# Optimization experiments

Measured on AMD Instinct MI355X. Metric: run time of the kernel, lower is better.

The kernel has to match this reference:

```python
import jax, jax.numpy as jnp
import numpy as np

PAD_IDX = 0
EPS = 1e-5


def make_pos(L):
    # phrase[i, j] = j - i, i.e. row i is range(-i, L-i)
    phrase = (np.arange(L)[None, :] - np.arange(L)[:, None]).astype(np.float32)
    half = int(np.ceil(L / 2))
    freq = np.linspace(0.0, L, L, dtype=np.float32)[1:half]          # [F]
    pos = freq[:, None, None] * phrase[None] / L * 2.0 * np.pi       # [F, L, L]
    pos = np.concatenate([np.cos(pos), np.sin(pos)], axis=0)        # [2F, L, L]
    return jnp.asarray(np.transpose(pos, (1, 0, 2)))                # [L, P=2F, L]


def setup_inputs() -> dict:
    key = jax.random.key(0)
    ks = jax.random.split(key, 8)
    B, L, V, D, H = 2048, 64, 4096, 64, 8
    P = 2 * (int(np.ceil(L / 2)) - 1)  # 62
    inputs = jax.random.randint(ks[0], (B, L), 0, V)
    W_emb = jax.random.normal(ks[1], (V, D), jnp.float32) * 0.02
    W_emb = W_emb.at[PAD_IDX].set(0.0)  # padding_idx row is zero
    W_qkv = jax.random.normal(ks[2], (3 * H * D, D), jnp.float32) * 0.02
    W_pos = jax.random.normal(ks[3], (P, L), jnp.float32) * 0.02
    ln_g = jnp.ones((D,), jnp.float32)
    ln_b = jnp.zeros((D,), jnp.float32)
    W1 = jax.random.normal(ks[4], (64, H), jnp.float32) * 0.1
    b1 = jnp.zeros((64,), jnp.float32)
    W2 = jax.random.normal(ks[5], (32, 64), jnp.float32) * 0.1
    b2 = jnp.zeros((32,), jnp.float32)
    return dict(inputs=inputs, W_emb=W_emb, W_qkv=W_qkv, W_pos=W_pos,
                ln_g=ln_g, ln_b=ln_b, W1=W1, b1=b1, W2=W2, b2=b2,
                n_words=4, n_names=16)


def reference(inputs, W_emb, W_qkv, W_pos, ln_g, ln_b, W1, b1, W2, b2, n_words, n_names):
    B, L = inputs.shape
    V, D = W_emb.shape
    H = W_qkv.shape[0] // (3 * D)
    pos = make_pos(L)  # [L, P, L]
    P = pos.shape[1]

    # compute_qkv: per-char q/k/v tables, then gather per token.
    qkv = (W_emb @ W_qkv.T).reshape(V, 3 * H, D)
    q, k, v = qkv[:, :H], qkv[:, H:2 * H], qkv[:, 2 * H:]
    q_t = jnp.take(q, inputs, axis=0)  # [B, L, H, D]
    k_t = jnp.take(k, inputs, axis=0)
    v_t = jnp.take(v, inputs, axis=0)

    # Equivalent to gathering char_sim[h, ids, ids]: qkv is a per-token linear,
    # so q[ids] @ k[ids]^T == char_sim.index_select(1, ids).index_select(-1, ids).
    sim = jnp.einsum('blhd,bmhd->bhlm', q_t, k_t) / jnp.sqrt(jnp.float32(D))
    key_pad = (inputs == PAD_IDX)[:, None, None, :]
    sim = jnp.where(key_pad, jnp.float32(-1e9), sim)  # char_sim[:, :, pad_idx] = -1e9

    # positional bias: Linear(L->P) on clipped scores, contracted with pos basis.
    sim_clip = jnp.where(sim > -1e8, sim, jnp.float32(0.0))
    pos_w = jnp.einsum('bhlm,pm->bhlp', sim_clip, W_pos)        # [B, H, L, P]
    pos_bias = jnp.einsum('bhlp,lpm->bhlm', pos_w, pos) / P     # mean over P

    attn = jax.nn.softmax(sim + pos_bias, axis=-1)              # dropout p=0 -> id
    out = jnp.einsum('bhlm,bmhd->blhd', attn, v_t)              # [B, L, H, D]

    # sdpa LayerNorm over word_vec_d
    mu = out.mean(-1, keepdims=True)
    var = out.var(-1, keepdims=True)
    out = (out - mu) * jax.lax.rsqrt(var + EPS) * ln_g + ln_b

    # MLP over the head dimension: [B, L, D, H] -> [B, L, D, 32]
    ft = jnp.swapaxes(out, 2, 3)
    h1 = jax.nn.relu(jnp.einsum('bldh,oh->bldo', ft, W1) + b1)
    h2 = jnp.einsum('bldo,po->bldp', h1, W2) + b2
    char_ft = h2.reshape(B, L, -1)                              # [B, L, D*32]

    # masked mean pooling over chars -> word feature
    maskf = (inputs != PAD_IDX).astype(char_ft.dtype)
    word_ft = jnp.einsum('bl,blf->bf', maskf, char_ft) / maskf.sum(-1, keepdims=True)

    # equal-size splits: words -> names (mean) -> groups of names
    Fdim = word_ft.shape[-1]
    name_ft = word_ft.reshape(B // n_words, n_words, Fdim).mean(1)
    return name_ft.reshape(-1, n_names, Fdim)
```

## Files before the change

### kernel.cpp

```cpp
#include <hip/hip_runtime.h>
#include <hip/hip_bf16.h>


typedef __attribute__((ext_vector_type(8))) short short8;
typedef __attribute__((ext_vector_type(4))) float f32x4;

union FragU { uint4 u; short8 v; };

__device__ __forceinline__ unsigned short f2bf(float f) {
    union { float f; unsigned int i; } c; c.f = f;
    unsigned int i = c.i;
    unsigned int r = (i + 0x7fffu + ((i >> 16) & 1u)) >> 16;
    return (unsigned short)r;
}
__device__ __forceinline__ float asf(unsigned int u) {
    union { unsigned int i; float f; } c; c.i = u; return c.f;
}
__device__ __forceinline__ float bfsel(uint2 g, int i) {
    unsigned u = (i < 2) ? g.x : g.y;
    return asf((i & 1) ? (u & 0xffff0000u) : (u << 16));
}
__device__ __forceinline__ unsigned cvtpk(float lo, float hi) {
    unsigned r;
    asm("v_cvt_pk_bf16_f32 %0, %1, %2" : "=v"(r) : "v"(lo), "v"(hi));
    return r;
}

__device__ __forceinline__ void packstore4(unsigned* rowptr, int c,
                                           float v0, float v1, float v2, float v3) {
    float p0 = __shfl_xor(v0, 1), p1 = __shfl_xor(v1, 1);
    float p2 = __shfl_xor(v2, 1), p3 = __shfl_xor(v3, 1);
    int odd = c & 1;
    float lo0 = odd ? p2 : v0, hi0 = odd ? v2 : p0;
    float lo1 = odd ? p3 : v1, hi1 = odd ? v3 : p1;
    unsigned a0 = cvtpk(lo0, hi0);
    unsigned a1 = cvtpk(lo1, hi1);
    int ba = (c >> 1) + (odd ? 16 : 0);
    rowptr[ba] = a0; rowptr[ba + 8] = a1;
}

__device__ __forceinline__ void packline(unsigned* rowbase, int c,
                                         float v0, float v1, float v2, float v3) {
    float p0 = __shfl_xor(v0, 1), p1 = __shfl_xor(v1, 1);
    float p2 = __shfl_xor(v2, 1), p3 = __shfl_xor(v3, 1);
    int odd = c & 1;
    float lo0 = odd ? p2 : v0, hi0 = odd ? v2 : p0;
    float lo1 = odd ? p3 : v1, hi1 = odd ? v3 : p1;
    unsigned a0 = cvtpk(lo0, hi0);
    unsigned a1 = cvtpk(lo1, hi1);
    int s = (c >> 1) + (odd ? 8 : 0);
    rowbase[s] = a0; rowbase[s + 16] = a1;
}

__global__ __launch_bounds__(256) void k_qkv(const float* __restrict__ W_emb,
                                             const float* __restrict__ W_qkv,
                                             unsigned short* __restrict__ qkvb) {
    __shared__ float At[4096];
    __shared__ float Bt[4096];
    int t = threadIdx.x;
    int bt = blockIdx.x / 24, rt = blockIdx.x - bt * 24;
    int r = t >> 2, part = t & 3;
    const float4* esrc = (const float4*)(W_emb + (size_t)((bt << 6) + r) * 64 + part * 16);
    const float4* wsrc = (const float4*)(W_qkv + (size_t)((rt << 6) + r) * 64 + part * 16);
#pragma unroll
    for (int j = 0; j < 4; ++j) {
        float4 e4 = esrc[j], w4 = wsrc[j];
        int c0 = part * 16 + j * 4;
        At[(c0 + 0) * 64 + r] = e4.x; At[(c0 + 1) * 64 + r] = e4.y;
        At[(c0 + 2) * 64 + r] = e4.z; At[(c0 + 3) * 64 + r] = e4.w;
        Bt[(c0 + 0) * 64 + r] = w4.x; Bt[(c0 + 1) * 64 + r] = w4.y;
        Bt[(c0 + 2) * 64 + r] = w4.z; Bt[(c0 + 3) * 64 + r] = w4.w;
    }
    __syncthreads();
    int l0 = (t >> 4) << 2, m0 = (t & 15) << 2;
    float acc[4][4] = {};
#pragma unroll 4
    for (int k = 0; k < 64; ++k) {
        float4 a  = *(const float4*)(At + k * 64 + l0);
        float4 bb = *(const float4*)(Bt + k * 64 + m0);
        float aa[4] = {a.x, a.y, a.z, a.w};
        float bv[4] = {bb.x, bb.y, bb.z, bb.w};
#pragma unroll
        for (int i = 0; i < 4; ++i)
#pragma unroll
            for (int j = 0; j < 4; ++j)
                acc[i][j] = fmaf(aa[i], bv[j], acc[i][j]);
    }
    float qs = (rt < 8) ? 0.18033688f : 1.0f;
#pragma unroll
    for (int i = 0; i < 4; ++i) {
        unsigned w0 = (unsigned)f2bf(acc[i][0] * qs) | ((unsigned)f2bf(acc[i][1] * qs) << 16);
        unsigned w1 = (unsigned)f2bf(acc[i][2] * qs) | ((unsigned)f2bf(acc[i][3] * qs) << 16);
        unsigned* dst = (unsigned*)(qkvb + (size_t)((bt << 6) + l0 + i) * 1536 + (rt << 6) + m0);
        dst[0] = w0; dst[1] = w1;
    }
}

__global__ void k_tab(const float* __restrict__ W_pos,
                      unsigned short* __restrict__ cst,
                      unsigned short* __restrict__ csl,
                      unsigned short* __restrict__ wpos) {
    int e = blockIdx.x * 256 + threadIdx.x;
    const float w = 6.283185307179586f / 63.0f;
    int row = e >> 6, col = e & 63;
    {
        int j = col, x = row;
        float val = 0.0f;
        if (j < 31)       val = cosf(w * (float)(((j + 1) * x) % 63));
        else if (j >= 32 && j < 63) val = sinf(w * (float)(((j - 31) * x) % 63));
        cst[e] = f2bf(val);
    }
    {
        int j = row, x = col;
        float val = 0.0f;
        if (j < 31)       val = cosf(w * (float)(((j + 1) * x) % 63));
        else if (j >= 32 && j < 63) val = sinf(w * (float)(((j - 31) * x) % 63));
        csl[e] = f2bf(val);
    }
    {
        int j = row;
        float val = 0.0f;
        if (j < 31) val = W_pos[j * 64 + col];
        else if (j >= 32 && j < 63) val = W_pos[(j - 1) * 64 + col];
        wpos[e] = f2bf(val);
    }
}

__global__ __launch_bounds__(128, 4) void k_attn(
    const int* __restrict__ inputs,
    const unsigned short* __restrict__ qkvb,
    const unsigned short* __restrict__ cstg,
    const unsigned short* __restrict__ cslg,
    const unsigned short* __restrict__ wposg,
    const float* __restrict__ ln_g,
    const float* __restrict__ ln_b,
    unsigned short* __restrict__ out_n)
{
    __shared__ __align__(16) unsigned int smem[4608];
    unsigned int* S0d = smem;
    unsigned int* S1d = smem + 2304;
    int t = threadIdx.x, w2 = t >> 6, lane = t & 63;
    int b = blockIdx.x >> 3, h = blockIdx.x & 7;
    const int* toks = inputs + b * 64;
    int r = lane & 15, q = lane >> 4, c = r;
    int tk = toks[lane];
    int mt0 = 2 * w2;
    const float INV62 = 1.0f / 62.0f;

    int mk[4]; float gvv[4], bvv[4];
#pragma unroll
    for (int nt = 0; nt < 4; ++nt) {
        mk[nt] = (toks[16 * nt + c] == 0);
        gvv[nt] = ln_g[16 * nt + c];
        bvv[nt] = ln_b[16 * nt + c];
    }

    {
        const uint4* src = (const uint4*)(qkvb + (size_t)tk * 1536 + (w2 ? 512 : 0) + h * 64);
        uint4* dst = (uint4*)((w2 ? S1d : S0d) + lane * 36);
#pragma unroll
        for (int j = 0; j < 8; ++j) dst[j] = src[j];
    }
    __syncthreads();

    f32x4 sc[2][4], acc[2][4];
    const f32x4 zf = {0.f, 0.f, 0.f, 0.f};

#pragma unroll
    for (int u = 0; u < 2; ++u)
#pragma unroll
        for (int nt = 0; nt < 4; ++nt) sc[u][nt] = zf;
#pragma unroll
    for (int ks = 0; ks < 2; ++ks) {
        FragU Af[2], Bf[4];
#pragma unroll
        for (int u = 0; u < 2; ++u)
            Af[u].u = *(const uint4*)(S0d + (16 * (mt0 + u) + r) * 36 + 16 * ks + 4 * q);
#pragma unroll
        for (int nt = 0; nt < 4; ++nt)
            Bf[nt].u = *(const uint4*)(S1d + (16 * nt + r) * 36 + 16 * ks + 4 * q);
#pragma unroll
        for (int u = 0; u < 2; ++u)
#pragma unroll
            for (int nt = 0; nt < 4; ++nt)
                sc[u][nt] = __builtin_amdgcn_mfma_f32_16x16x32_bf16(Af[u].v, Bf[nt].v, sc[u][nt], 0, 0, 0);
    }
#pragma unroll
    for (int u = 0; u < 2; ++u)
#pragma unroll
        for (int i = 0; i < 4; ++i) {
            int l = 16 * (mt0 + u) + 4 * q + i;
            packstore4(S0d + l * 36, c, sc[u][0][i], sc[u][1][i], sc[u][2][i], sc[u][3][i]);
        }
    __syncthreads();

#pragma unroll
    for (int u = 0; u < 2; ++u)
#pragma unroll
        for (int nt = 0; nt < 4; ++nt) acc[u][nt] = zf;
#pragma unroll
    for (int ks = 0; ks < 2; ++ks) {
        FragU Af[2], Bf[4];
#pragma unroll
        for (int u = 0; u < 2; ++u)
            Af[u].u = *(const uint4*)(S0d + (16 * (mt0 + u) + r) * 36 + 16 * ks + 4 * q);
#pragma unroll
        for (int nt = 0; nt < 4; ++nt)
            Bf[nt].u = *(const uint4*)(wposg + (16 * nt + r) * 64 + 32 * ks + 8 * q);
#pragma unroll
        for (int u = 0; u < 2; ++u)
#pragma unroll
            for (int nt = 0; nt < 4; ++nt)
                acc[u][nt] = __builtin_amdgcn_mfma_f32_16x16x32_bf16(Af[u].v, Bf[nt].v, acc[u][nt], 0, 0, 0);
    }
#pragma unroll
    for (int u = 0; u < 2; ++u) {
        int mt = mt0 + u;
        uint2 t00 = *(const uint2*)(cslg + (c) * 64 + 16 * mt + 4 * q);
        uint2 t01 = *(const uint2*)(cslg + (32 + c) * 64 + 16 * mt + 4 * q);
        uint2 t10 = *(const uint2*)(cslg + (16 + c) * 64 + 16 * mt + 4 * q);
        uint2 t11 = *(const uint2*)(cslg + (48 + c) * 64 + 16 * mt + 4 * q);
#pragma unroll
        for (int i = 0; i < 4; ++i) {
            int l = 16 * mt + 4 * q + i;
            float cv0 = bfsel(t00, i), sv0 = bfsel(t01, i);
            float cv1 = bfsel(t10, i), sv1 = bfsel(t11, i);
            float pc0 = acc[u][0][i], ps0 = acc[u][2][i];
            float pc1 = acc[u][1][i], ps1 = acc[u][3][i];
            float u0 = pc0 * cv0 - ps0 * sv0;
            float u1 = pc1 * cv1 - ps1 * sv1;
            float u2 = pc0 * sv0 + ps0 * cv0;
            float u3 = pc1 * sv1 + ps1 * cv1;
            packstore4(S1d + l * 36, c, u0, u1, u2, u3);
        }
    }

#pragma unroll
    for (int u = 0; u < 2; ++u)
#pragma unroll
        for (int nt = 0; nt < 4; ++nt) acc[u][nt] = zf;
#pragma unroll
    for (int ks = 0; ks < 2; ++ks) {
        FragU Af[2], Bf[4];
#pragma unroll
        for (int u = 0; u < 2; ++u)
            Af[u].u = *(const uint4*)(S1d + (16 * (mt0 + u) + r) * 36 + 16 * ks + 4 * q);
#pragma unroll
        for (int nt = 0; nt < 4; ++nt)
            Bf[nt].u = *(const uint4*)(cstg + (16 * nt + r) * 64 + 32 * ks + 8 * q);
#pragma unroll
        for (int u = 0; u < 2; ++u)
#pragma unroll
            for (int nt = 0; nt < 4; ++nt)
                acc[u][nt] = __builtin_amdgcn_mfma_f32_16x16x32_bf16(Af[u].v, Bf[nt].v, acc[u][nt], 0, 0, 0);
    }

    uint4 V4[4];
    {
        const uint4* vsrc = (const uint4*)(qkvb + (size_t)tk * 1536 + 1024 + h * 64 + 32 * w2);
#pragma unroll
        for (int j = 0; j < 4; ++j) V4[j] = vsrc[j];
    }

#pragma unroll
    for (int u = 0; u < 2; ++u)
#pragma unroll
        for (int i = 0; i < 4; ++i) {
            int l = 16 * (mt0 + u) + 4 * q + i;
            float e0 = mk[0] ? 0.f : __builtin_amdgcn_exp2f(fmaf(acc[u][0][i], INV62, sc[u][0][i]));
            float e1 = mk[1] ? 0.f : __builtin_amdgcn_exp2f(fmaf(acc[u][1][i], INV62, sc[u][1][i]));
            float e2 = mk[2] ? 0.f : __builtin_amdgcn_exp2f(fmaf(acc[u][2][i], INV62, sc[u][2][i]));
            float e3 = mk[3] ? 0.f : __builtin_amdgcn_exp2f(fmaf(acc[u][3][i], INV62, sc[u][3][i]));
            float s = e0 + e1 + e2 + e3;
            s += __shfl_xor(s, 1);
            s += __shfl_xor(s, 2);
            s += __shfl_xor(s, 4);
            s += __shfl_xor(s, 8);
            float inv = __builtin_amdgcn_rcpf(s);
            packstore4(S0d + l * 36, c, e0 * inv, e1 * inv, e2 * inv, e3 * inv);
        }

    {
        int odd = lane & 1;
        const unsigned* Vd = (const unsigned*)V4;
#pragma unroll
        for (int jj = 0; jj < 16; ++jj) {
            unsigned my = Vd[jj];
            unsigned pr = __shfl_xor(my, 1);
            unsigned val = odd ? ((pr >> 16) | (my & 0xffff0000u))
                               : ((my & 0xffffu) | (pr << 16));
            S1d[(32 * w2 + 2 * jj + odd) * 36 + (lane >> 1)] = val;
        }
    }
    __syncthreads();

#pragma unroll
    for (int u = 0; u < 2; ++u)
#pragma unroll
        for (int nt = 0; nt < 4; ++nt) acc[u][nt] = zf;
#pragma unroll
    for (int ks = 0; ks < 2; ++ks) {
        FragU Af[2], Bf[4];
#pragma unroll
        for (int u = 0; u < 2; ++u)
            Af[u].u = *(const uint4*)(S0d + (16 * (mt0 + u) + r) * 36 + 16 * ks + 4 * q);
#pragma unroll
        for (int nt = 0; nt < 4; ++nt)
            Bf[nt].u = *(const uint4*)(S1d + (16 * nt + r) * 36 + 16 * ks + 4 * q);
#pragma unroll
        for (int u = 0; u < 2; ++u)
#pragma unroll
            for (int nt = 0; nt < 4; ++nt)
                acc[u][nt] = __builtin_amdgcn_mfma_f32_16x16x32_bf16(Af[u].v, Bf[nt].v, acc[u][nt], 0, 0, 0);
    }
    {
        unsigned* outw = (unsigned*)out_n;
        size_t hb = ((size_t)b * 8 + h) * 64;
#pragma unroll
        for (int u = 0; u < 2; ++u)
#pragma unroll
            for (int i = 0; i < 4; ++i) {
                int l = 16 * (mt0 + u) + 4 * q + i;
                float v0 = acc[u][0][i], v1 = acc[u][1][i], v2 = acc[u][2][i], v3 = acc[u][3][i];
                float s1 = v0 + v1 + v2 + v3;
                float s2 = v0 * v0 + v1 * v1 + v2 * v2 + v3 * v3;
                s1 += __shfl_xor(s1, 1); s2 += __shfl_xor(s2, 1);
                s1 += __shfl_xor(s1, 2); s2 += __shfl_xor(s2, 2);
                s1 += __shfl_xor(s1, 4); s2 += __shfl_xor(s2, 4);
                s1 += __shfl_xor(s1, 8); s2 += __shfl_xor(s2, 8);
                float mu = s1 * (1.0f / 64.0f);
                float var = s2 * (1.0f / 64.0f) - mu * mu;
                float rstd = __builtin_amdgcn_rsqf(var + 1e-5f);
                float cmu = -mu * rstd;
                float y0 = fmaf(fmaf(v0, rstd, cmu), gvv[0], bvv[0]);
                float y1 = fmaf(fmaf(v1, rstd, cmu), gvv[1], bvv[1]);
                float y2 = fmaf(fmaf(v2, rstd, cmu), gvv[2], bvv[2]);
                float y3 = fmaf(fmaf(v3, rstd, cmu), gvv[3], bvv[3]);
                packline(outw + (hb + l) * 32, c, y0, y1, y2, y3);
            }
    }
}

__global__ __launch_bounds__(256) void k_mlp(const int* __restrict__ inputs,
                                             const unsigned short* __restrict__ out_n,
                                             const float* __restrict__ W1,
                                             const float* __restrict__ b1,
                                             float* __restrict__ gws) {
    __shared__ unsigned short XT[8320];
    __shared__ unsigned long long vmask_s;
    __shared__ float invcnt_s;
    int t = threadIdx.x, w = t >> 6, lane = t & 63;
    int b = blockIdx.x;
    int ot = w >> 1, dt = w & 1;
    int kq = lane >> 4, n = lane & 15;

    if (t < 64) {
        int tok = inputs[b * 64 + t];
        unsigned long long bal = __ballot(tok != 0);
        if (t == 0) {
            int cnt = __popcll(bal);
            if (cnt < 1) cnt = 1;
            vmask_s = bal;
            invcnt_s = 1.0f / (float)cnt;
        }
    }

    FragU Wf[2];
#pragma unroll
    for (int om = 0; om < 2; ++om) {
        int o = 32 * ot + 16 * om + n;
        if (kq == 0) {
            const float4* wsrc = (const float4*)(W1 + o * 8);
            float4 wa = wsrc[0], wb = wsrc[1];
            Wf[om].u.x = (unsigned)f2bf(wa.x) | ((unsigned)f2bf(wa.y) << 16);
            Wf[om].u.y = (unsigned)f2bf(wa.z) | ((unsigned)f2bf(wa.w) << 16);
            Wf[om].u.z = (unsigned)f2bf(wb.x) | ((unsigned)f2bf(wb.y) << 16);
            Wf[om].u.w = (unsigned)f2bf(wb.z) | ((unsigned)f2bf(wb.w) << 16);
        } else if (kq == 1) {
            Wf[om].u = make_uint4((unsigned)f2bf(b1[o]), 0, 0, 0);
        } else {
            Wf[om].u = make_uint4(0, 0, 0, 0);
        }
    }

    f32x4 racc[2][2];
    const f32x4 zf = {0.f, 0.f, 0.f, 0.f};
#pragma unroll
    for (int dm = 0; dm < 2; ++dm)
#pragma unroll
        for (int om = 0; om < 2; ++om) racc[dm][om] = zf;

    int lh = t & 7;
    int lr = (t >> 3) & 15;
    int half = t >> 7;

    const uint4* src4 = (const uint4*)(out_n + (size_t)b * 32768 + lh * 4096
                                       + lr * 64 + half * 32);
    uint4 G[4], Gn[4];
#pragma unroll
    for (int j = 0; j < 4; ++j) G[j] = src4[j];

    int c2 = lh >> 1, lodd = lh & 1;
    unsigned* XTd = (unsigned*)XT;
    int dbase = lr * 260 + c2;

    __syncthreads();
    unsigned long long vmask = vmask_s;
    float invcnt = invcnt_s;

    for (int cc = 0; cc < 4; ++cc) {
        __syncthreads();
#pragma unroll
        for (int j = 0; j < 4; ++j) {
            int m0 = half * 32 + j * 8;
            int d0 = (m0 >= 16 && m0 < 48) ? (m0 ^ 48) : m0;
            unsigned wv[4] = {G[j].x, G[j].y, G[j].z, G[j].w};
#pragma unroll
            for (int i = 0; i < 4; ++i) {
                unsigned pw = __shfl_xor(wv[i], 1);
                unsigned val = lodd ? ((pw >> 16) | (wv[i] & 0xffff0000u))
                                    : ((wv[i] & 0xffffu) | (pw << 16));
                int d = d0 + 2 * i + lodd;
                XTd[dbase + d * 4] = val;
            }
        }
        if (cc < 3) {
#pragma unroll
            for (int j = 0; j < 4; ++j) Gn[j] = src4[(cc + 1) * 128 + j];
        }
        __syncthreads();
#pragma unroll 4
        for (int l = 0; l < 16; ++l) {
            if (!((vmask >> (16 * cc + l)) & 1ull)) continue;
            FragU Xf[2];
#pragma unroll
            for (int dm = 0; dm < 2; ++dm) {
                if (kq == 0)
                    Xf[dm].u = *(const uint4*)(XT + l * 520 + (32 * dt + 16 * dm + n) * 8);
                else if (kq == 1)
                    Xf[dm].u = make_uint4(0x3F80u, 0, 0, 0);
                else
                    Xf[dm].u = make_uint4(0, 0, 0, 0);
            }
#pragma unroll
            for (int dm = 0; dm < 2; ++dm)
#pragma unroll
                for (int om = 0; om < 2; ++om) {
                    f32x4 C = __builtin_amdgcn_mfma_f32_16x16x32_bf16(Xf[dm].v, Wf[om].v, zf, 0, 0, 0);
#pragma unroll
                    for (int i = 0; i < 4; ++i)
                        racc[dm][om][i] += fmaxf(C[i], 0.0f);
                }
        }
        if (cc < 3) {
#pragma unroll
            for (int j = 0; j < 4; ++j) G[j] = Gn[j];
        }
    }
    float* gb = gws + (size_t)b * 4096;
#pragma unroll
    for (int dm = 0; dm < 2; ++dm)
#pragma unroll
        for (int om = 0; om < 2; ++om) {
            int o = 32 * ot + 16 * om + n;
#pragma unroll
            for (int i = 0; i < 4; ++i) {
                int d = 32 * dt + 16 * dm + 4 * kq + i;
                gb[d * 64 + o] = racc[dm][om][i] * invcnt;
            }
        }
}

__global__ __launch_bounds__(256) void k_final(const float* __restrict__ gws,
                                               const float* __restrict__ W2,
                                               const float* __restrict__ b2,
                                               float* __restrict__ out) {
    __shared__ float gbar[4096];
    __shared__ float w2s[32 * 68];
    __shared__ float b2s[32];
    int t = threadIdx.x;
    int n = blockIdx.x;
    for (int e = t; e < 4096; e += 256) {
        size_t base = (size_t)(4 * n) * 4096 + e;
        gbar[e] = 0.25f * (gws[base] + gws[base + 4096] + gws[base + 8192] + gws[base + 12288]);
    }
    for (int e = t; e < 2048; e += 256) {
        int p = e >> 6, o = e & 63;
        w2s[p * 68 + o] = W2[e];
    }
    if (t < 32) b2s[t] = b2[t];
    __syncthreads();
#pragma unroll
    for (int jj = 0; jj < 8; ++jj) {
        int f = jj * 256 + t;
        int d = f >> 5, p = f & 31;
        float acc = b2s[p];
        for (int o4 = 0; o4 < 16; ++o4) {
            float4 gvv = *(const float4*)(gbar + d * 64 + o4 * 4);
            float4 wv = *(const float4*)(w2s + p * 68 + o4 * 4);
            acc = fmaf(gvv.x, wv.x, acc);
            acc = fmaf(gvv.y, wv.y, acc);
            acc = fmaf(gvv.z, wv.z, acc);
            acc = fmaf(gvv.w, wv.w, acc);
        }
        out[(size_t)n * 2048 + f] = acc;
    }
}

extern "C" void kernel_launch(void* const* d_in, const int* in_sizes, int n_in,
                              void* d_out, int out_size, void* d_ws, size_t ws_size,
                              hipStream_t stream) {
    const int*   inputs = (const int*)d_in[0];
    const float* W_emb  = (const float*)d_in[1];
    const float* W_qkv  = (const float*)d_in[2];
    const float* W_pos  = (const float*)d_in[3];
    const float* ln_g   = (const float*)d_in[4];
    const float* ln_b   = (const float*)d_in[5];
    const float* W1     = (const float*)d_in[6];
    const float* b1     = (const float*)d_in[7];
    const float* W2     = (const float*)d_in[8];
    const float* b2     = (const float*)d_in[9];
    float* out = (float*)d_out;

    unsigned short* qkvb = (unsigned short*)d_ws;
    unsigned short* cst  = qkvb + 6291456;
    unsigned short* csl  = cst + 4096;
    unsigned short* wpos = csl + 4096;
    float* gws = (float*)(wpos + 4096);
    unsigned short* out_n = (unsigned short*)(gws + 8388608);

    hipLaunchKernelGGL(k_qkv,   dim3(64 * 24), dim3(256), 0, stream, W_emb, W_qkv, qkvb);
    hipLaunchKernelGGL(k_tab,   dim3(16),      dim3(256), 0, stream, W_pos, cst, csl, wpos);
    hipLaunchKernelGGL(k_attn,  dim3(16384),   dim3(128), 0, stream,
                       inputs, qkvb, cst, csl, wpos, ln_g, ln_b, out_n);
    hipLaunchKernelGGL(k_mlp,   dim3(2048),    dim3(256), 0, stream, inputs, out_n, W1, b1, gws);
    hipLaunchKernelGGL(k_final, dim3(512),     dim3(256), 0, stream, gws, W2, b2, out);
}
```

Measured before the change: 350.2 us.

## Split attention block across four waves, one 16-row tile per wave

The attention kernel now launches 256 threads per block instead of 128, so each of four waves handles one 16-row M tile rather than two. The Q/K staging load is redistributed over all 256 threads, and each wave loads and transposes only a 16-column slice of V. This halves per-wave accumulator registers and doubles the waves available for latency hiding. In exchange, every wave reloads the same B fragments from LDS and global tables, and barriers now synchronise more waves.

```diff
diff --git a/kernel.cpp b/kernel.cpp
--- a/kernel.cpp
+++ b/kernel.cpp
@@ -126,7 +126,7 @@
     }
 }
 
-__global__ __launch_bounds__(128, 4) void k_attn(
+__global__ __launch_bounds__(256, 8) void k_attn(
     const int* __restrict__ inputs,
     const unsigned short* __restrict__ qkvb,
     const unsigned short* __restrict__ cstg,
@@ -139,12 +139,12 @@
     __shared__ __align__(16) unsigned int smem[4608];
     unsigned int* S0d = smem;
     unsigned int* S1d = smem + 2304;
-    int t = threadIdx.x, w2 = t >> 6, lane = t & 63;
+    int t = threadIdx.x, w4 = t >> 6, lane = t & 63;
     int b = blockIdx.x >> 3, h = blockIdx.x & 7;
     const int* toks = inputs + b * 64;
     int r = lane & 15, q = lane >> 4, c = r;
     int tk = toks[lane];
-    int mt0 = 2 * w2;
+    int mt = w4;
     const float INV62 = 1.0f / 62.0f;
 
     int mk[4]; float gvv[4], bvv[4];
@@ -156,66 +156,55 @@
     }
 
     {
-        const uint4* src = (const uint4*)(qkvb + (size_t)tk * 1536 + (w2 ? 512 : 0) + h * 64);
-        uint4* dst = (uint4*)((w2 ? S1d : S0d) + lane * 36);
-#pragma unroll
-        for (int j = 0; j < 8; ++j) dst[j] = src[j];
+        int isK = t >> 7;
+        int row = (t >> 1) & 63;
+        int half = t & 1;
+        int tkr = toks[row];
+        const uint4* src = (const uint4*)(qkvb + (size_t)tkr * 1536 + (isK ? 512 : 0)
+                                          + h * 64 + half * 32);
+        uint4* dst = (uint4*)((isK ? S1d : S0d) + row * 36) + half * 4;
+#pragma unroll
+        for (int j = 0; j < 4; ++j) dst[j] = src[j];
     }
     __syncthreads();
 
-    f32x4 sc[2][4], acc[2][4];
+    f32x4 sc[4], acc[4];
     const f32x4 zf = {0.f, 0.f, 0.f, 0.f};
 
 #pragma unroll
-    for (int u = 0; u < 2; ++u)
-#pragma unroll
-        for (int nt = 0; nt < 4; ++nt) sc[u][nt] = zf;
+    for (int nt = 0; nt < 4; ++nt) sc[nt] = zf;
 #pragma unroll
     for (int ks = 0; ks < 2; ++ks) {
-        FragU Af[2], Bf[4];
-#pragma unroll
-        for (int u = 0; u < 2; ++u)
-            Af[u].u = *(const uint4*)(S0d + (16 * (mt0 + u) + r) * 36 + 16 * ks + 4 * q);
+        FragU Af, Bf[4];
+        Af.u = *(const uint4*)(S0d + (16 * mt + r) * 36 + 16 * ks + 4 * q);
 #pragma unroll
         for (int nt = 0; nt < 4; ++nt)
             Bf[nt].u = *(const uint4*)(S1d + (16 * nt + r) * 36 + 16 * ks + 4 * q);
 #pragma unroll
-        for (int u = 0; u < 2; ++u)
-#pragma unroll
-            for (int nt = 0; nt < 4; ++nt)
-                sc[u][nt] = __builtin_amdgcn_mfma_f32_16x16x32_bf16(Af[u].v, Bf[nt].v, sc[u][nt], 0, 0, 0);
-    }
-#pragma unroll
-    for (int u = 0; u < 2; ++u)
-#pragma unroll
-        for (int i = 0; i < 4; ++i) {
-            int l = 16 * (mt0 + u) + 4 * q + i;
-            packstore4(S0d + l * 36, c, sc[u][0][i], sc[u][1][i], sc[u][2][i], sc[u][3][i]);
-        }
+        for (int nt = 0; nt < 4; ++nt)
+            sc[nt] = __builtin_amdgcn_mfma_f32_16x16x32_bf16(Af.v, Bf[nt].v, sc[nt], 0, 0, 0);
+    }
+#pragma unroll
+    for (int i = 0; i < 4; ++i) {
+        int l = 16 * mt + 4 * q + i;
+        packstore4(S0d + l * 36, c, sc[0][i], sc[1][i], sc[2][i], sc[3][i]);
+    }
     __syncthreads();
 
 #pragma unroll
-    for (int u = 0; u < 2; ++u)
-#pragma unroll
-        for (int nt = 0; nt < 4; ++nt) acc[u][nt] = zf;
+    for (int nt = 0; nt < 4; ++nt) acc[nt] = zf;
 #pragma unroll
     for (int ks = 0; ks < 2; ++ks) {
-        FragU Af[2], Bf[4];
-#pragma unroll
-        for (int u = 0; u < 2; ++u)
-            Af[u].u = *(const uint4*)(S0d + (16 * (mt0 + u) + r) * 36 + 16 * ks + 4 * q);
+        FragU Af, Bf[4];
+        Af.u = *(const uint4*)(S0d + (16 * mt + r) * 36 + 16 * ks + 4 * q);
 #pragma unroll
         for (int nt = 0; nt < 4; ++nt)
             Bf[nt].u = *(const uint4*)(wposg + (16 * nt + r) * 64 + 32 * ks + 8 * q);
 #pragma unroll
-        for (int u = 0; u < 2; ++u)
-#pragma unroll
-            for (int nt = 0; nt < 4; ++nt)
-                acc[u][nt] = __builtin_amdgcn_mfma_f32_16x16x32_bf16(Af[u].v, Bf[nt].v, acc[u][nt], 0, 0, 0);
-    }
-#pragma unroll
-    for (int u = 0; u < 2; ++u) {
-        int mt = mt0 + u;
+        for (int nt = 0; nt < 4; ++nt)
+            acc[nt] = __builtin_amdgcn_mfma_f32_16x16x32_bf16(Af.v, Bf[nt].v, acc[nt], 0, 0, 0);
+    }
+    {
         uint2 t00 = *(const uint2*)(cslg + (c) * 64 + 16 * mt + 4 * q);
         uint2 t01 = *(const uint2*)(cslg + (32 + c) * 64 + 16 * mt + 4 * q);
         uint2 t10 = *(const uint2*)(cslg + (16 + c) * 64 + 16 * mt + 4 * q);
@@ -225,8 +214,8 @@
             int l = 16 * mt + 4 * q + i;
             float cv0 = bfsel(t00, i), sv0 = bfsel(t01, i);
             float cv1 = bfsel(t10, i), sv1 = bfsel(t11, i);
-            float pc0 = acc[u][0][i], ps0 = acc[u][2][i];
-            float pc1 = acc[u][1][i], ps1 = acc[u][3][i];
+            float pc0 = acc[0][i], ps0 = acc[2][i];
+            float pc1 = acc[1][i], ps1 = acc[3][i];
             float u0 = pc0 * cv0 - ps0 * sv0;
             float u1 = pc1 * cv1 - ps1 * sv1;
             float u2 = pc0 * sv0 + ps0 * cv0;
@@ -236,108 +225,91 @@
     }
 
 #pragma unroll
-    for (int u = 0; u < 2; ++u)
-#pragma unroll
-        for (int nt = 0; nt < 4; ++nt) acc[u][nt] = zf;
+    for (int nt = 0; nt < 4; ++nt) acc[nt] = zf;
 #pragma unroll
     for (int ks = 0; ks < 2; ++ks) {
-        FragU Af[2], Bf[4];
-#pragma unroll
-        for (int u = 0; u < 2; ++u)
-            Af[u].u = *(const uint4*)(S1d + (16 * (mt0 + u) + r) * 36 + 16 * ks + 4 * q);
+        FragU Af, Bf[4];
+        Af.u = *(const uint4*)(S1d + (16 * mt + r) * 36 + 16 * ks + 4 * q);
 #pragma unroll
         for (int nt = 0; nt < 4; ++nt)
             Bf[nt].u = *(const uint4*)(cstg + (16 * nt + r) * 64 + 32 * ks + 8 * q);
 #pragma unroll
-        for (int u = 0; u < 2; ++u)
-#pragma unroll
-            for (int nt = 0; nt < 4; ++nt)
-                acc[u][nt] = __builtin_amdgcn_mfma_f32_16x16x32_bf16(Af[u].v, Bf[nt].v, acc[u][nt], 0, 0, 0);
-    }
-
-    uint4 V4[4];
-    {
-        const uint4* vsrc = (const uint4*)(qkvb + (size_t)tk * 1536 + 1024 + h * 64 + 32 * w2);
-#pragma unroll
-        for (int j = 0; j < 4; ++j) V4[j] = vsrc[j];
-    }
-
-#pragma unroll
-    for (int u = 0; u < 2; ++u)
-#pragma unroll
-        for (int i = 0; i < 4; ++i) {
-            int l = 16 * (mt0 + u) + 4 * q + i;
-            float e0 = mk[0] ? 0.f : __builtin_amdgcn_exp2f(fmaf(acc[u][0][i], INV62, sc[u][0][i]));
-            float e1 = mk[1] ? 0.f : __builtin_amdgcn_exp2f(fmaf(acc[u][1][i], INV62, sc[u][1][i]));
-            float e2 = mk[2] ? 0.f : __builtin_amdgcn_exp2f(fmaf(acc[u][2][i], INV62, sc[u][2][i]));
-            float e3 = mk[3] ? 0.f : __builtin_amdgcn_exp2f(fmaf(acc[u][3][i], INV62, sc[u][3][i]));
-            float s = e0 + e1 + e2 + e3;
-            s += __shfl_xor(s, 1);
-            s += __shfl_xor(s, 2);
-            s += __shfl_xor(s, 4);
-            s += __shfl_xor(s, 8);
-            float inv = __builtin_amdgcn_rcpf(s);
-            packstore4(S0d + l * 36, c, e0 * inv, e1 * inv, e2 * inv, e3 * inv);
-        }
+        for (int nt = 0; nt < 4; ++nt)
+            acc[nt] = __builtin_amdgcn_mfma_f32_16x16x32_bf16(Af.v, Bf[nt].v, acc[nt], 0, 0, 0);
+    }
+
+    uint4 V4[2];
+    {
+        const uint4* vsrc = (const uint4*)(qkvb + (size_t)tk * 1536 + 1024 + h * 64 + 16 * w4);
+        V4[0] = vsrc[0]; V4[1] = vsrc[1];
+    }
+
+#pragma unroll
+    for (int i = 0; i < 4; ++i) {
+        int l = 16 * mt + 4 * q + i;
+        float e0 = mk[0] ? 0.f : __builtin_amdgcn_exp2f(fmaf(acc[0][i], INV62, sc[0][i]));
+        float e1 = mk[1] ? 0.f : __builtin_amdgcn_exp2f(fmaf(acc[1][i], INV62, sc[1][i]));
+        float e2 = mk[2] ? 0.f : __builtin_amdgcn_exp2f(fmaf(acc[2][i], INV62, sc[2][i]));
+        float e3 = mk[3] ? 0.f : __builtin_amdgcn_exp2f(fmaf(acc[3][i], INV62, sc[3][i]));
+        float s = e0 + e1 + e2 + e3;
+        s += __shfl_xor(s, 1);
+        s += __shfl_xor(s, 2);
+        s += __shfl_xor(s, 4);
+        s += __shfl_xor(s, 8);
+        float inv = __builtin_amdgcn_rcpf(s);
+        packstore4(S0d + l * 36, c, e0 * inv, e1 * inv, e2 * inv, e3 * inv);
+    }
 
     {
         int odd = lane & 1;
         const unsigned* Vd = (const unsigned*)V4;
 #pragma unroll
-        for (int jj = 0; jj < 16; ++jj) {
+        for (int jj = 0; jj < 8; ++jj) {
             unsigned my = Vd[jj];
             unsigned pr = __shfl_xor(my, 1);
             unsigned val = odd ? ((pr >> 16) | (my & 0xffff0000u))
                                : ((my & 0xffffu) | (pr << 16));
-            S1d[(32 * w2 + 2 * jj + odd) * 36 + (lane >> 1)] = val;
+            S1d[(16 * w4 + 2 * jj + odd) * 36 + (lane >> 1)] = val;
         }
     }
     __syncthreads();
 
 #pragma unroll
-    for (int u = 0; u < 2; ++u)
-#pragma unroll
-        for (int nt = 0; nt < 4; ++nt) acc[u][nt] = zf;
+    for (int nt = 0; nt < 4; ++nt) acc[nt] = zf;
 #pragma unroll
     for (int ks = 0; ks < 2; ++ks) {
-        FragU Af[2], Bf[4];
-#pragma unroll
-        for (int u = 0; u < 2; ++u)
-            Af[u].u = *(const uint4*)(S0d + (16 * (mt0 + u) + r) * 36 + 16 * ks + 4 * q);
+        FragU Af, Bf[4];
+        Af.u = *(const uint4*)(S0d + (16 * mt + r) * 36 + 16 * ks + 4 * q);
 #pragma unroll
         for (int nt = 0; nt < 4; ++nt)
             Bf[nt].u = *(const uint4*)(S1d + (16 * nt + r) * 36 + 16 * ks + 4 * q);
 #pragma unroll
-        for (int u = 0; u < 2; ++u)
-#pragma unroll
-            for (int nt = 0; nt < 4; ++nt)
-                acc[u][nt] = __builtin_amdgcn_mfma_f32_16x16x32_bf16(Af[u].v, Bf[nt].v, acc[u][nt], 0, 0, 0);
+        for (int nt = 0; nt < 4; ++nt)
+            acc[nt] = __builtin_amdgcn_mfma_f32_16x16x32_bf16(Af.v, Bf[nt].v, acc[nt], 0, 0, 0);
     }
     {
         unsigned* outw = (unsigned*)out_n;
         size_t hb = ((size_t)b * 8 + h) * 64;
 #pragma unroll
-        for (int u = 0; u < 2; ++u)
-#pragma unroll
-            for (int i = 0; i < 4; ++i) {
-                int l = 16 * (mt0 + u) + 4 * q + i;
-                float v0 = acc[u][0][i], v1 = acc[u][1][i], v2 = acc[u][2][i], v3 = acc[u][3][i];
-                float s1 = v0 + v1 + v2 + v3;
-                float s2 = v0 * v0 + v1 * v1 + v2 * v2 + v3 * v3;
-                s1 += __shfl_xor(s1, 1); s2 += __shfl_xor(s2, 1);
-                s1 += __shfl_xor(s1, 2); s2 += __shfl_xor(s2, 2);
-                s1 += __shfl_xor(s1, 4); s2 += __shfl_xor(s2, 4);
-                s1 += __shfl_xor(s1, 8); s2 += __shfl_xor(s2, 8);
-                float mu = s1 * (1.0f / 64.0f);
-                float var = s2 * (1.0f / 64.0f) - mu * mu;
-                float rstd = __builtin_amdgcn_rsqf(var + 1e-5f);
-                float cmu = -mu * rstd;
-                float y0 = fmaf(fmaf(v0, rstd, cmu), gvv[0], bvv[0]);
-                float y1 = fmaf(fmaf(v1, rstd, cmu), gvv[1], bvv[1]);
-                float y2 = fmaf(fmaf(v2, rstd, cmu), gvv[2], bvv[2]);
-                float y3 = fmaf(fmaf(v3, rstd, cmu), gvv[3], bvv[3]);
-                packline(outw + (hb + l) * 32, c, y0, y1, y2, y3);
-            }
+        for (int i = 0; i < 4; ++i) {
+            int l = 16 * mt + 4 * q + i;
+            float v0 = acc[0][i], v1 = acc[1][i], v2 = acc[2][i], v3 = acc[3][i];
+            float s1 = v0 + v1 + v2 + v3;
+            float s2 = v0 * v0 + v1 * v1 + v2 * v2 + v3 * v3;
+            s1 += __shfl_xor(s1, 1); s2 += __shfl_xor(s2, 1);
+            s1 += __shfl_xor(s1, 2); s2 += __shfl_xor(s2, 2);
+            s1 += __shfl_xor(s1, 4); s2 += __shfl_xor(s2, 4);
+            s1 += __shfl_xor(s1, 8); s2 += __shfl_xor(s2, 8);
+            float mu = s1 * (1.0f / 64.0f);
+            float var = s2 * (1.0f / 64.0f) - mu * mu;
+            float rstd = __builtin_amdgcn_rsqf(var + 1e-5f);
+            float cmu = -mu * rstd;
+            float y0 = fmaf(fmaf(v0, rstd, cmu), gvv[0], bvv[0]);
+            float y1 = fmaf(fmaf(v1, rstd, cmu), gvv[1], bvv[1]);
+            float y2 = fmaf(fmaf(v2, rstd, cmu), gvv[2], bvv[2]);
+            float y3 = fmaf(fmaf(v3, rstd, cmu), gvv[3], bvv[3]);
+            packline(outw + (hb + l) * 32, c, y0, y1, y2, y3);
+        }
     }
 }
 
@@ -531,7 +503,7 @@
 
     hipLaunchKernelGGL(k_qkv,   dim3(64 * 24), dim3(256), 0, stream, W_emb, W_qkv, qkvb);
     hipLaunchKernelGGL(k_tab,   dim3(16),      dim3(256), 0, stream, W_pos, cst, csl, wpos);
-    hipLaunchKernelGGL(k_attn,  dim3(16384),   dim3(128), 0, stream,
+    hipLaunchKernelGGL(k_attn,  dim3(16384),   dim3(256), 0, stream,
                        inputs, qkvb, cst, csl, wpos, ln_g, ln_b, out_n);
     hipLaunchKernelGGL(k_mlp,   dim3(2048),    dim3(256), 0, stream, inputs, out_n, W1, b1, gws);
     hipLaunchKernelGGL(k_final, dim3(512),     dim3(256), 0, stream, gws, W2, b2, out);
```

Result: slower. 438.3 us (+25.2%).
